# Kernel optimization log

Measured on AMD Instinct MI355X. Metric: run time of the kernel, lower is better.

Reference implementation:

```python
import jax, jax.numpy as jnp
from jax import lax
import numpy as np

B, T, N, F_IN, H, E, K = 8, 32, 500, 64, 128, 8000, 3
LN_EPS = 1e-5


def setup_inputs() -> dict:
    key = jax.random.key(0)
    ks = jax.random.split(key, 10)
    x = jax.random.normal(ks[0], (B, T, N, F_IN), dtype=jnp.float32)
    edge_index = jax.random.randint(ks[1], (2, E), 0, N, dtype=jnp.int64)
    edge_weight = jax.random.uniform(ks[2], (E,), dtype=jnp.float32)
    # GCNConv: linear (in->out) + bias
    W_gcn = jax.random.normal(ks[3], (F_IN, H), dtype=jnp.float32) / np.sqrt(F_IN)
    b_gcn = jnp.zeros((H,), dtype=jnp.float32)
    # Conv1d(H, H, K): weight (O, I, K)
    W_temp = jax.random.normal(ks[4], (H, H, K), dtype=jnp.float32) / np.sqrt(H * K)
    b_temp = jnp.zeros((H,), dtype=jnp.float32)
    # LayerNorm(H)
    ln_w = jnp.ones((H,), dtype=jnp.float32)
    ln_b = jnp.zeros((H,), dtype=jnp.float32)
    # residual Linear (in->out)
    W_res = jax.random.normal(ks[5], (F_IN, H), dtype=jnp.float32) / np.sqrt(F_IN)
    b_res = jnp.zeros((H,), dtype=jnp.float32)
    return {"x": x, "edge_index": edge_index, "edge_weight": edge_weight,
            "W_gcn": W_gcn, "b_gcn": b_gcn, "W_temp": W_temp, "b_temp": b_temp,
            "ln_w": ln_w, "ln_b": ln_b, "W_res": W_res, "b_res": b_res}


def reference(x, edge_index, edge_weight, W_gcn, b_gcn, W_temp, b_temp, ln_w, ln_b, W_res, b_res):
    Bv, Tv, Nv, Fv = x.shape
    Hv = W_gcn.shape[1]
    res = x @ W_res + b_res  # (B,T,N,H)

    # ---- spatial GCNConv on B*T replicated graphs (vectorized, no index offsetting) ----
    xf = x.reshape(Bv * Tv, Nv, Fv) @ W_gcn  # (BT,N,H)
    src, dst = edge_index[0], edge_index[1]
    loops = jnp.arange(Nv, dtype=edge_index.dtype)
    src2 = jnp.concatenate([src, loops])
    dst2 = jnp.concatenate([dst, loops])
    ew2 = jnp.concatenate([edge_weight, jnp.ones((Nv,), dtype=edge_weight.dtype)])
    deg = jax.ops.segment_sum(ew2, dst2, num_segments=Nv)
    dinv = jnp.where(deg > 0, deg ** -0.5, 0.0)
    norm = dinv[src2] * ew2 * dinv[dst2]  # (E+N,)
    msgs = xf[:, src2, :] * norm[None, :, None]  # (BT, E+N, H)
    agg = jax.vmap(lambda m: jax.ops.segment_sum(m, dst2, num_segments=Nv))(msgs)
    h = jax.nn.gelu(agg + b_gcn, approximate=False)  # (BT,N,H)

    # ---- temporal Conv1d over T ----
    h = h.reshape(Bv, Tv, Nv, Hv).transpose(0, 2, 3, 1).reshape(Bv * Nv, Hv, Tv)
    pad = K // 2
    h = lax.conv_general_dilated(h, W_temp, window_strides=(1,), padding=[(pad, pad)],
                                 dimension_numbers=("NCH", "OIH", "NCH"))
    h = jax.nn.gelu(h + b_temp[None, :, None], approximate=False)
    h = h.reshape(Bv, Nv, Hv, Tv).transpose(0, 3, 1, 2)  # (B,T,N,H)

    # ---- fused residual + LayerNorm over last dim ----
    y = h + res
    mu = jnp.mean(y, axis=-1, keepdims=True)
    var = jnp.mean((y - mu) ** 2, axis=-1, keepdims=True)
    return (y - mu) * lax.rsqrt(var + LN_EPS) * ln_w + ln_b
```

## Files before the change

kernel.cpp:

```cpp
#include <hip/hip_runtime.h>
#include <hip/hip_bf16.h>
#include <math.h>

#define Bv 8
#define Tv 32
#define Nv 500
#define Fin 64
#define Hv 128
#define Ev 8000
#define Kv 3
#define BT (Bv*Tv)
#define ROWS (BT*Nv)
#define KK (Kv*Hv)

#define HROW 136
#define ZROW (32*HROW)
#define AGS_BASE (ZROW+HROW)
#define AGROW 72
#define SMEM_SHORTS (AGS_BASE + 32*AGROW)

typedef __attribute__((ext_vector_type(8))) short s8v;
typedef __attribute__((ext_vector_type(4))) float f4v;

__device__ __forceinline__ float gelu_exact(float v){
    float t  = v*0.70710678118654752440f;
    float ax = fabsf(t);
    float k  = __builtin_amdgcn_rcpf(fmaf(0.3275911f, ax, 1.0f));
    float p  = k*fmaf(k, fmaf(k, fmaf(k, fmaf(k, 1.061405429f, -1.453152027f),
                                      1.421413741f), -0.284496736f), 0.254829592f);
    float e  = __expf(-ax*ax);
    float er = fmaf(-p, e, 1.0f);
    er = copysignf(er, t);
    return 0.5f*v*(1.0f + er);
}
__device__ __forceinline__ short f2bs(float f){
    union { __hip_bfloat16 h; short s; } u;
    u.h = __float2bfloat16(f);
    return u.s;
}
__device__ __forceinline__ float b2f(short s){
    union { unsigned int i; float f; } u;
    u.i = ((unsigned int)(unsigned short)s) << 16;
    return u.f;
}

__global__ __launch_bounds__(1024) void k_xprep(const float* __restrict__ x,
        short* __restrict__ X2b, const float* __restrict__ W,
        const float* __restrict__ Wg, const float* __restrict__ Wr,
        short* __restrict__ W2, short* __restrict__ Wgt, short* __restrict__ Wrt,
        const int* __restrict__ ei, const float* __restrict__ ew,
        float* __restrict__ dinv, int* __restrict__ offs,
        int* __restrict__ csrc, float* __restrict__ cw){
    __shared__ float sdeg[Nv];
    __shared__ int   scnt[Nv];
    __shared__ float sdv[Nv];
    __shared__ int   scur[Nv];
    __shared__ int   sa[512], sb[512];
    int bid = blockIdx.x;
    int tid = threadIdx.x;
    if (bid == 0){
        if (tid < Nv){ sdeg[tid] = 1.0f; scnt[tid] = 0; }
        __syncthreads();
        for (int e = tid; e < Ev; e += 1024){
            int d = ei[Ev + e];
            atomicAdd(&sdeg[d], ew[e]);
            atomicAdd(&scnt[d], 1);
        }
        __syncthreads();
        int c = 0;
        if (tid < Nv){
            float d = sdeg[tid];
            float v = (d > 0.f) ? rsqrtf(d) : 0.f;
            sdv[tid] = v; dinv[tid] = v;
        }
        if (tid < 512){ c = (tid < Nv) ? scnt[tid] : 0; sa[tid] = c; }
        __syncthreads();
        int* s = sa; int* t = sb;
        for (int off = 1; off < 512; off <<= 1){
            int v = 0;
            if (tid < 512){ v = s[tid]; if (tid >= off) v += s[tid - off]; }
            if (tid < 512) t[tid] = v;
            __syncthreads();
            int* tmp = s; s = t; t = tmp;
        }
        if (tid < Nv){ int excl = s[tid] - c; offs[tid] = excl; scur[tid] = excl; }
        if (tid == 0) offs[Nv] = Ev;
        __syncthreads();
        for (int e = tid; e < Ev; e += 1024){
            int sn = ei[e], d = ei[Ev + e];
            int pos = atomicAdd(&scur[d], 1);
            csrc[pos] = sn;
            cw[pos] = sdv[sn]*ew[e]*sdv[d];
        }
    } else if (bid <= ROWS/64){
        int gid = (bid-1)*1024 + tid;
        int row = gid >> 4, c4 = gid & 15;
        int bt = row / Nv;
        int n  = row - bt*Nv;
        float4 v = ((const float4*)x)[gid];
        short4 sv;
        sv.x = f2bs(v.x); sv.y = f2bs(v.y); sv.z = f2bs(v.z); sv.w = f2bs(v.w);
        *(short4*)(X2b + (size_t)n*(BT*64) + bt*64 + c4*4) = sv;
    } else {
        int idx = (bid - 1 - ROWS/64)*1024 + tid;
        if (idx < Hv*Hv*Kv){
            int o = idx/(Hv*Kv);
            int rem = idx - o*(Hv*Kv);
            int i = rem/Kv, k = rem - i*Kv;
            W2[o*KK + k*Hv + i] = f2bs(W[idx]);
        } else if (idx < Hv*Hv*Kv + Hv*64){
            int j = idx - Hv*Hv*Kv;
            int o = j >> 6, k = j & 63;
            Wgt[j] = f2bs(Wg[k*Hv + o]);
        } else if (idx < Hv*Hv*Kv + 2*Hv*64){
            int j = idx - Hv*Hv*Kv - Hv*64;
            int o = j >> 6, k = j & 63;
            Wrt[j] = f2bs(Wr[k*Hv + o]);
        }
    }
}

__global__ __launch_bounds__(256, 2) void k_mega(
        const short* __restrict__ X2b,
        const float* __restrict__ dinv, const int* __restrict__ offs,
        const int* __restrict__ csrc, const float* __restrict__ cw,
        const short* __restrict__ W2, const short* __restrict__ Wgt,
        const short* __restrict__ Wrt,
        const float* __restrict__ bg, const float* __restrict__ btm,
        const float* __restrict__ br, const float* __restrict__ lw,
        const float* __restrict__ lb, float* __restrict__ out){
    __shared__ short smem[SMEM_SHORTS];
    float (*red)[4][2] = (float(*)[4][2])&smem[AGS_BASE];
    int tid  = threadIdx.x;
    int w    = tid >> 6;
    int lane = tid & 63;
    int quad = lane >> 4;
    int laneo = lane & 15;
    int bid = blockIdx.x;
    int b  = bid & 7;
    int n  = bid >> 3;
    int o_base = w*32;

    float bgv[2], bbv[2], brv[2], lwv[2], lbv[2];
    #pragma unroll
    for (int nt = 0; nt < 2; ++nt){
        int o = o_base + nt*16 + laneo;
        bgv[nt] = bg[o]; bbv[nt] = btm[o]; brv[nt] = br[o];
        lwv[nt] = lw[o]; lbv[nt] = lb[o];
    }

    if (tid < 16){
        s8v z = {0,0,0,0,0,0,0,0};
        *(s8v*)&smem[ZROW + tid*8] = z;
    }

    {
        int tr = tid >> 3;
        int c8 = tid & 7;
        int woff = b*2048 + tid*8;
        float dv = dinv[n];
        float sw = dv*dv;
        float a4[4][8];
        s8v v = *(const s8v*)(X2b + (size_t)n*(BT*64) + woff);
        #pragma unroll
        for (int q = 0; q < 8; ++q){
            a4[0][q] = sw * b2f(v[q]);
            a4[1][q] = 0.f; a4[2][q] = 0.f; a4[3][q] = 0.f;
        }
        int e0 = offs[n], e1 = offs[n+1];
        for (int base = e0; base < e1; base += 4){
            int sn[4]; float wv[4];
            #pragma unroll
            for (int j = 0; j < 4; ++j){
                int idx = base + j;
                bool p = idx < e1;
                sn[j] = p ? csrc[idx] : n;
                wv[j] = p ? cw[idx] : 0.f;
            }
            s8v u[4];
            #pragma unroll
            for (int j = 0; j < 4; ++j)
                u[j] = *(const s8v*)(X2b + (size_t)sn[j]*(BT*64) + woff);
            #pragma unroll
            for (int j = 0; j < 4; ++j)
                #pragma unroll
                for (int q = 0; q < 8; ++q)
                    a4[j][q] = fmaf(wv[j], b2f(u[j][q]), a4[j][q]);
        }
        s8v rr;
        #pragma unroll
        for (int q = 0; q < 8; ++q)
            rr[q] = f2bs((a4[0][q] + a4[1][q]) + (a4[2][q] + a4[3][q]));
        *(s8v*)&smem[AGS_BASE + tr*AGROW + c8*8] = rr;
    }

    s8v bwg[2][2];
    #pragma unroll
    for (int nt = 0; nt < 2; ++nt){
        const short* wp = Wgt + (o_base + nt*16 + laneo)*64 + quad*8;
        bwg[nt][0] = *(const s8v*)wp;
        bwg[nt][1] = *(const s8v*)(wp + 32);
    }
    __syncthreads();

    #pragma unroll
    for (int m = 0; m < 2; ++m){
        const short* arp = &smem[AGS_BASE + (m*16 + laneo)*AGROW + quad*8];
        s8v a0 = *(const s8v*)arp;
        s8v a1 = *(const s8v*)(arp + 32);
        f4v h0 = {0.f,0.f,0.f,0.f}, h1 = {0.f,0.f,0.f,0.f};
        h0 = __builtin_amdgcn_mfma_f32_16x16x32_bf16(a0, bwg[0][0], h0, 0,0,0);
        h0 = __builtin_amdgcn_mfma_f32_16x16x32_bf16(a1, bwg[0][1], h0, 0,0,0);
        h1 = __builtin_amdgcn_mfma_f32_16x16x32_bf16(a0, bwg[1][0], h1, 0,0,0);
        h1 = __builtin_amdgcn_mfma_f32_16x16x32_bf16(a1, bwg[1][1], h1, 0,0,0);
        #pragma unroll
        for (int r = 0; r < 4; ++r){
            int t = m*16 + quad*4 + r;
            short* hrow = &smem[t*HROW];
            hrow[o_base + laneo]      = f2bs(gelu_exact(h0[r] + bgv[0]));
            hrow[o_base + 16 + laneo] = f2bs(gelu_exact(h1[r] + bgv[1]));
        }
    }

    s8v breg[2][12], bwr[2][2];
    #pragma unroll
    for (int nt = 0; nt < 2; ++nt){
        int o = o_base + nt*16 + laneo;
        const short* wp = W2 + o*KK + quad*8;
        #pragma unroll
        for (int s = 0; s < 12; ++s)
            breg[nt][s] = *(const s8v*)(wp + s*32);
        const short* wr = Wrt + o*64 + quad*8;
        bwr[nt][0] = *(const s8v*)wr;
        bwr[nt][1] = *(const s8v*)(wr + 32);
    }
    __syncthreads();

    f4v acc[2][2];
    #pragma unroll
    for (int m = 0; m < 2; ++m)
        #pragma unroll
        for (int nt = 0; nt < 2; ++nt)
            acc[m][nt] = (f4v){0.f,0.f,0.f,0.f};
    #pragma unroll
    for (int m = 0; m < 2; ++m){
        #pragma unroll
        for (int s = 0; s < 12; ++s){
            int k  = s >> 2;
            int i0 = (s & 3) * 32;
            int row = m*16 + laneo + k - 1;
            int hb = ((unsigned)row > 31u) ? ZROW : row*HROW;
            s8v a = *(const s8v*)&smem[hb + i0 + quad*8];
            acc[m][0] = __builtin_amdgcn_mfma_f32_16x16x32_bf16(a, breg[0][s], acc[m][0], 0,0,0);
            acc[m][1] = __builtin_amdgcn_mfma_f32_16x16x32_bf16(a, breg[1][s], acc[m][1], 0,0,0);
        }
    }
    f4v racc[2][2];
    #pragma unroll
    for (int m = 0; m < 2; ++m)
        #pragma unroll
        for (int nt = 0; nt < 2; ++nt)
            racc[m][nt] = (f4v){0.f,0.f,0.f,0.f};
    const short* xp = X2b + ((size_t)n*BT + b*Tv)*64;
    #pragma unroll
    for (int m = 0; m < 2; ++m){
        const short* xrp = xp + (m*16 + laneo)*64 + quad*8;
        s8v a0 = *(const s8v*)xrp;
        s8v a1 = *(const s8v*)(xrp + 32);
        racc[m][0] = __builtin_amdgcn_mfma_f32_16x16x32_bf16(a0, bwr[0][0], racc[m][0], 0,0,0);
        racc[m][0] = __builtin_amdgcn_mfma_f32_16x16x32_bf16(a1, bwr[0][1], racc[m][0], 0,0,0);
        racc[m][1] = __builtin_amdgcn_mfma_f32_16x16x32_bf16(a0, bwr[1][0], racc[m][1], 0,0,0);
        racc[m][1] = __builtin_amdgcn_mfma_f32_16x16x32_bf16(a1, bwr[1][1], racc[m][1], 0,0,0);
    }
    size_t obase = ((size_t)b*Tv*Nv + n)*Hv;
    float yv[2][2][4];
    float srow[2][4], ssrow[2][4];
    #pragma unroll
    for (int m = 0; m < 2; ++m)
        #pragma unroll
        for (int r = 0; r < 4; ++r){ srow[m][r] = 0.f; ssrow[m][r] = 0.f; }
    #pragma unroll
    for (int m = 0; m < 2; ++m){
        #pragma unroll
        for (int nt = 0; nt < 2; ++nt){
            #pragma unroll
            for (int r = 0; r < 4; ++r){
                float gv = gelu_exact(acc[m][nt][r] + bbv[nt]);
                float y = gv + racc[m][nt][r] + brv[nt];
                yv[m][nt][r] = y;
                srow[m][r] += y; ssrow[m][r] += y*y;
            }
        }
    }
    #pragma unroll
    for (int m = 0; m < 2; ++m)
        #pragma unroll
        for (int r = 0; r < 4; ++r){
            #pragma unroll
            for (int msk = 8; msk >= 1; msk >>= 1){
                srow[m][r]  += __shfl_xor(srow[m][r],  msk, 64);
                ssrow[m][r] += __shfl_xor(ssrow[m][r], msk, 64);
            }
        }
    if (laneo == 0){
        #pragma unroll
        for (int m = 0; m < 2; ++m)
            #pragma unroll
            for (int r = 0; r < 4; ++r){
                int t = m*16 + quad*4 + r;
                red[t][w][0] = srow[m][r];
                red[t][w][1] = ssrow[m][r];
            }
    }
    __syncthreads();
    #pragma unroll
    for (int m = 0; m < 2; ++m){
        #pragma unroll
        for (int r = 0; r < 4; ++r){
            int t = m*16 + quad*4 + r;
            float s  = red[t][0][0] + red[t][1][0] + red[t][2][0] + red[t][3][0];
            float ss = red[t][0][1] + red[t][1][1] + red[t][2][1] + red[t][3][1];
            float mu = s * (1.f/128.f);
            float var = fmaxf(ss * (1.f/128.f) - mu*mu, 0.f);
            float rstd = rsqrtf(var + 1e-5f);
            #pragma unroll
            for (int nt = 0; nt < 2; ++nt){
                int o = o_base + nt*16 + laneo;
                out[obase + (size_t)t*Nv*Hv + o] =
                    (yv[m][nt][r] - mu)*rstd*lwv[nt] + lbv[nt];
            }
        }
    }
}

extern "C" void kernel_launch(void* const* d_in, const int* in_sizes, int n_in,
                              void* d_out, int out_size, void* d_ws, size_t ws_size,
                              hipStream_t stream){
    const float* x   = (const float*)d_in[0];
    const int*   ei  = (const int*)d_in[1];
    const float* ew  = (const float*)d_in[2];
    const float* Wg  = (const float*)d_in[3];
    const float* bg  = (const float*)d_in[4];
    const float* Wtm = (const float*)d_in[5];
    const float* btm = (const float*)d_in[6];
    const float* lw  = (const float*)d_in[7];
    const float* lb  = (const float*)d_in[8];
    const float* Wr  = (const float*)d_in[9];
    const float* br  = (const float*)d_in[10];
    float* out = (float*)d_out;

    char* ws = (char*)d_ws;
    float* dinv = (float*)(ws + 0);
    int*   offs = (int*)  (ws + 4096);
    int*   csrc = (int*)  (ws + 8192);
    float* cwn  = (float*)(ws + 40960);
    short* W2   = (short*)(ws + 73728);
    short* Wgt  = (short*)(ws + 172032);
    short* Wrt  = (short*)(ws + 188416);
    short* X2b  = (short*)(ws + 204800);

    k_xprep<<<1 + ROWS/64 + 64, 1024, 0, stream>>>(x, X2b, Wtm, Wg, Wr,
                                                   W2, Wgt, Wrt,
                                                   ei, ew, dinv, offs, csrc, cwn);
    k_mega <<<8*Nv, 256, 0, stream>>>(X2b, dinv, offs, csrc, cwn,
                                      W2, Wgt, Wrt,
                                      bg, btm, br, lw, lb, out);
}
```

Measured before the change: 218.5 us.

## Stream conv weights per tap to cut registers and raise occupancy to 3

Instead of preloading all 24 bf16 weight fragments for the temporal conv into registers before the barrier, the kernel now loads the 8 fragments for one tap per iteration of a non-unrolled k loop. Launch bounds move from 2 to 3 blocks per SIMD-occupancy hint to use the freed registers. The residual-input loads are hoisted ahead of the conv loop so their latency overlaps it. The trade-off is that weight loads now sit on the critical path inside the loop, which the extra occupancy is meant to hide.

```diff
diff --git a/kernel.cpp b/kernel.cpp
--- a/kernel.cpp
+++ b/kernel.cpp
@@ -120,7 +120,7 @@
     }
 }
 
-__global__ __launch_bounds__(256, 2) void k_mega(
+__global__ __launch_bounds__(256, 3) void k_mega(
         const short* __restrict__ X2b,
         const float* __restrict__ dinv, const int* __restrict__ offs,
         const int* __restrict__ csrc, const float* __restrict__ cw,
@@ -222,37 +222,52 @@
         }
     }
 
-    s8v breg[2][12], bwr[2][2];
+    s8v bwr[2][2];
     #pragma unroll
     for (int nt = 0; nt < 2; ++nt){
-        int o = o_base + nt*16 + laneo;
-        const short* wp = W2 + o*KK + quad*8;
-        #pragma unroll
-        for (int s = 0; s < 12; ++s)
-            breg[nt][s] = *(const s8v*)(wp + s*32);
-        const short* wr = Wrt + o*64 + quad*8;
+        const short* wr = Wrt + (o_base + nt*16 + laneo)*64 + quad*8;
         bwr[nt][0] = *(const s8v*)wr;
         bwr[nt][1] = *(const s8v*)(wr + 32);
     }
     __syncthreads();
 
+    s8v xa[2][2];
+    {
+        const short* xp = X2b + ((size_t)n*BT + b*Tv)*64;
+        #pragma unroll
+        for (int m = 0; m < 2; ++m){
+            const short* xrp = xp + (m*16 + laneo)*64 + quad*8;
+            xa[m][0] = *(const s8v*)xrp;
+            xa[m][1] = *(const s8v*)(xrp + 32);
+        }
+    }
+
     f4v acc[2][2];
     #pragma unroll
     for (int m = 0; m < 2; ++m)
         #pragma unroll
         for (int nt = 0; nt < 2; ++nt)
             acc[m][nt] = (f4v){0.f,0.f,0.f,0.f};
-    #pragma unroll
-    for (int m = 0; m < 2; ++m){
-        #pragma unroll
-        for (int s = 0; s < 12; ++s){
-            int k  = s >> 2;
-            int i0 = (s & 3) * 32;
+    #pragma unroll 1
+    for (int k = 0; k < 3; ++k){
+        s8v bsl[2][4];
+        #pragma unroll
+        for (int nt = 0; nt < 2; ++nt){
+            const short* wp = W2 + (o_base + nt*16 + laneo)*KK + k*128 + quad*8;
+            #pragma unroll
+            for (int j = 0; j < 4; ++j)
+                bsl[nt][j] = *(const s8v*)(wp + j*32);
+        }
+        #pragma unroll
+        for (int m = 0; m < 2; ++m){
             int row = m*16 + laneo + k - 1;
             int hb = ((unsigned)row > 31u) ? ZROW : row*HROW;
-            s8v a = *(const s8v*)&smem[hb + i0 + quad*8];
-            acc[m][0] = __builtin_amdgcn_mfma_f32_16x16x32_bf16(a, breg[0][s], acc[m][0], 0,0,0);
-            acc[m][1] = __builtin_amdgcn_mfma_f32_16x16x32_bf16(a, breg[1][s], acc[m][1], 0,0,0);
+            #pragma unroll
+            for (int j = 0; j < 4; ++j){
+                s8v a = *(const s8v*)&smem[hb + j*32 + quad*8];
+                acc[m][0] = __builtin_amdgcn_mfma_f32_16x16x32_bf16(a, bsl[0][j], acc[m][0], 0,0,0);
+                acc[m][1] = __builtin_amdgcn_mfma_f32_16x16x32_bf16(a, bsl[1][j], acc[m][1], 0,0,0);
+            }
         }
     }
     f4v racc[2][2];
@@ -261,16 +276,12 @@
         #pragma unroll
         for (int nt = 0; nt < 2; ++nt)
             racc[m][nt] = (f4v){0.f,0.f,0.f,0.f};
-    const short* xp = X2b + ((size_t)n*BT + b*Tv)*64;
     #pragma unroll
     for (int m = 0; m < 2; ++m){
-        const short* xrp = xp + (m*16 + laneo)*64 + quad*8;
-        s8v a0 = *(const s8v*)xrp;
-        s8v a1 = *(const s8v*)(xrp + 32);
-        racc[m][0] = __builtin_amdgcn_mfma_f32_16x16x32_bf16(a0, bwr[0][0], racc[m][0], 0,0,0);
-        racc[m][0] = __builtin_amdgcn_mfma_f32_16x16x32_bf16(a1, bwr[0][1], racc[m][0], 0,0,0);
-        racc[m][1] = __builtin_amdgcn_mfma_f32_16x16x32_bf16(a0, bwr[1][0], racc[m][1], 0,0,0);
-        racc[m][1] = __builtin_amdgcn_mfma_f32_16x16x32_bf16(a1, bwr[1][1], racc[m][1], 0,0,0);
+        racc[m][0] = __builtin_amdgcn_mfma_f32_16x16x32_bf16(xa[m][0], bwr[0][0], racc[m][0], 0,0,0);
+        racc[m][0] = __builtin_amdgcn_mfma_f32_16x16x32_bf16(xa[m][1], bwr[0][1], racc[m][0], 0,0,0);
+        racc[m][1] = __builtin_amdgcn_mfma_f32_16x16x32_bf16(xa[m][0], bwr[1][0], racc[m][1], 0,0,0);
+        racc[m][1] = __builtin_amdgcn_mfma_f32_16x16x32_bf16(xa[m][1], bwr[1][1], racc[m][1], 0,0,0);
     }
     size_t obase = ((size_t)b*Tv*Nv + n)*Hv;
     float yv[2][2][4];
```

Result: faster. 208.9 us (-4.4%).
